# Kernel tuning notes

Hardware: AMD Instinct MI355X
Metric: run time of the kernel (lower is better)

Reference implementation:

```python
import jax, jax.numpy as jnp
import numpy as np
import math

def setup_inputs() -> dict:
    key = jax.random.key(0)
    k1, k2, k3 = jax.random.split(key, 3)
    B, N, C = 32, 1024, 768
    x = jax.random.normal(k1, (B, N, C), dtype=jnp.float32)
    W = jax.random.normal(k2, (4, C), dtype=jnp.float32) * 0.02  # conv1x1 weight [out=4, in=C]
    b = jax.random.normal(k3, (4,), dtype=jnp.float32) * 0.02
    return {"x": x, "W": W, "b": b}

def reference(x, W, b):
    B, N, C = x.shape
    H = int(math.isqrt(N))
    L = H * H
    # [B,N,C] -> [B,C,H,H]
    xi = jnp.transpose(x, (0, 2, 1)).reshape(B, C, H, H)
    # alpha = Conv1x1(AvgPool(x)) -> [B,4]
    pooled = jnp.mean(xi, axis=(2, 3))                      # [B,C]
    alpha = pooled @ W.T + b                                # [B,4]
    a = alpha[:, :, None, None]                             # [B,4,1,1]
    # CrossScan directions
    x0 = xi.reshape(B, C, L)                                # row-major scan
    x1 = jnp.transpose(xi, (0, 1, 3, 2)).reshape(B, C, L)   # col-major scan
    x2 = x0[:, :, ::-1]                                     # reversed row-major
    x3 = x1[:, :, ::-1]                                     # reversed col-major
    # gated weighted sum over the 4 scans (fused elementwise)
    y = a[:, 0] * x0 + a[:, 1] * x1 + a[:, 2] * x2 + a[:, 3] * x3  # [B,C,L]
    return jnp.transpose(y, (0, 2, 1))                      # [B,L,C]
```

## Files before the change

### kernel.cpp

```cpp
#include <hip/hip_runtime.h>

#define BB 32
#define NN 1024
#define CC 768
#define HH 32
#define NCHUNK 32
#define NPER (NN / NCHUNK)
#define C4 (CC / 4)
#define NORB 272
#define OPB 4
#define MBLK (NORB / OPB)

typedef float f32x4 __attribute__((ext_vector_type(4)));

__global__ void pool_dot(const f32x4* __restrict__ x4,
                         const f32x4* __restrict__ W4,
                         f32x4* __restrict__ partW4) {
    const int blk = blockIdx.x;
    const int t   = threadIdx.x;
    const f32x4* xb = x4 + (size_t)blk * (NPER * C4) + t;
    f32x4 s = {0.f, 0.f, 0.f, 0.f};
#pragma unroll 8
    for (int n = 0; n < NPER; ++n) s += xb[(size_t)n * C4];

    float d[4];
#pragma unroll
    for (int k = 0; k < 4; ++k) {
        const f32x4 w = W4[k * C4 + t];
        d[k] = s.x * w.x + s.y * w.y + s.z * w.z + s.w * w.w;
    }
    const int lane = t & 63;
    const int wid  = t >> 6;
    __shared__ float red[3][4];
#pragma unroll
    for (int k = 0; k < 4; ++k) {
        float v = d[k];
#pragma unroll
        for (int off = 32; off >= 1; off >>= 1) v += __shfl_down(v, off);
        if (lane == 0) red[wid][k] = v;
    }
    __syncthreads();
    if (t == 0) {
        f32x4 w;
        w.x = red[0][0] + red[1][0] + red[2][0];
        w.y = red[0][1] + red[1][1] + red[2][1];
        w.z = red[0][2] + red[1][2] + red[2][2];
        w.w = red[0][3] + red[1][3] + red[2][3];
        partW4[blk] = w;
    }
}

__global__ void merge(const f32x4* __restrict__ x4,
                      const f32x4* __restrict__ partW4,
                      const f32x4* __restrict__ bias4,
                      f32x4* __restrict__ o4) {
    const int bidx = blockIdx.x;
    const int b = bidx / MBLK;
    const int j = bidx - b * MBLK;

    f32x4 acc = {0.f, 0.f, 0.f, 0.f};
#pragma unroll 8
    for (int ch = 0; ch < NCHUNK; ++ch) acc += partW4[b * NCHUNK + ch];
    const f32x4 al = acc * (1.0f / (float)NN) + bias4[0];
    const float a0 = al.x, a1 = al.y, a2 = al.z, a3 = al.w;

    const int t = threadIdx.x;
    const f32x4* xb = x4 + (size_t)b * (NN * C4);
    f32x4* ob = o4 + (size_t)b * (NN * C4);

    int L[OPB][4];
#pragma unroll
    for (int q = 0; q < OPB; ++q) {
        const int o = OPB * j + q;
        int r = 0;
#pragma unroll
        for (int rr = 1; rr <= 15; ++rr) if (rr * (33 - rr) <= o) r = rr;
        const int c = r + (o - r * (33 - r));
        L[q][0] = r * HH + c;
        L[q][1] = c * HH + r;
        L[q][2] = (NN - 1) - L[q][0];
        L[q][3] = (NN - 1) - L[q][1];
    }

    f32x4 v[OPB][4];
#pragma unroll
    for (int q = 0; q < OPB; ++q)
#pragma unroll
        for (int m = 0; m < 4; ++m)
            v[q][m] = xb[(size_t)L[q][m] * C4 + t];

#pragma unroll
    for (int q = 0; q < OPB; ++q) {
        __builtin_nontemporal_store(a0 * v[q][0] + a1 * v[q][1] + a2 * v[q][2] + a3 * v[q][3],
                                    &ob[(size_t)L[q][0] * C4 + t]);
        __builtin_nontemporal_store(a0 * v[q][1] + a1 * v[q][0] + a2 * v[q][3] + a3 * v[q][2],
                                    &ob[(size_t)L[q][1] * C4 + t]);
        __builtin_nontemporal_store(a0 * v[q][2] + a1 * v[q][3] + a2 * v[q][0] + a3 * v[q][1],
                                    &ob[(size_t)L[q][2] * C4 + t]);
        __builtin_nontemporal_store(a0 * v[q][3] + a1 * v[q][2] + a2 * v[q][1] + a3 * v[q][0],
                                    &ob[(size_t)L[q][3] * C4 + t]);
    }
}

extern "C" void kernel_launch(void* const* d_in, const int* in_sizes, int n_in,
                              void* d_out, int out_size, void* d_ws, size_t ws_size,
                              hipStream_t stream) {
    const float* x    = (const float*)d_in[0];
    const float* W    = (const float*)d_in[1];
    const float* bias = (const float*)d_in[2];
    float* out = (float*)d_out;

    f32x4* partW = (f32x4*)d_ws;

    pool_dot<<<BB * NCHUNK, 192, 0, stream>>>((const f32x4*)x, (const f32x4*)W, partW);
    merge<<<BB * MBLK, 192, 0, stream>>>((const f32x4*)x, partW,
                                         (const f32x4*)bias, (f32x4*)out);
}
```

Measured before the change: 195.3 us.

## Fuse pooling and merge into one cooperative kernel holding x in registers

Replaces the two-kernel pool-then-merge pipeline with a single cooperative kernel. Each block loads its 32 rows of x into registers, computes partial pooled dot products, does a grid-wide sync, then writes the gated outputs from the registers it already holds. This halves global reads of x and removes one kernel launch. The costs are a grid barrier, high register pressure for 32 float4 values per thread, and an occupancy requirement (checked at runtime, with a fallback to the old path).

```diff
diff --git a/kernel.cpp b/kernel.cpp
--- a/kernel.cpp
+++ b/kernel.cpp
@@ -1,17 +1,129 @@
 #include <hip/hip_runtime.h>
+#include <hip/hip_cooperative_groups.h>
+
+namespace cg = cooperative_groups;
 
 #define BB 32
 #define NN 1024
 #define CC 768
 #define HH 32
+#define C4 (CC / 4)
+#define NTHR 192
+#define QPB 8
+#define BLKB 32
+#define GRID (BB * BLKB)
 #define NCHUNK 32
 #define NPER (NN / NCHUNK)
-#define C4 (CC / 4)
 #define NORB 272
 #define OPB 4
 #define MBLK (NORB / OPB)
 
 typedef float f32x4 __attribute__((ext_vector_type(4)));
+
+__device__ __forceinline__ void quad_rows(int jb, int u, int& r0, int& r1, int& r2, int& r3) {
+    if (jb < 30) {
+        const int q = jb * QPB + u;
+        int r = 0;
+#pragma unroll
+        for (int rr = 1; rr <= 14; ++rr) if (rr * (31 - rr) <= q) r = rr;
+        const int c = (r + 1) + (q - r * (31 - r));
+        r0 = r * HH + c;
+        r1 = c * HH + r;
+        r2 = (NN - 1) - r0;
+        r3 = (NN - 1) - r1;
+    } else {
+        const int i = (jb - 30) * QPB + u;
+        r0 = 33 * i;
+        r1 = 1023 - 33 * i;
+        r2 = 31 * (i + 1);
+        r3 = 992 - 31 * i;
+    }
+}
+
+__global__ __launch_bounds__(NTHR, 3) void fused(const f32x4* __restrict__ x4,
+                                                 const f32x4* __restrict__ W4,
+                                                 const f32x4* __restrict__ bias4,
+                                                 f32x4* __restrict__ partW4,
+                                                 f32x4* __restrict__ o4) {
+    const int blk = blockIdx.x;
+    const int b   = blk >> 5;
+    const int jb  = blk & 31;
+    const int t   = threadIdx.x;
+
+    const f32x4* xb = x4 + (size_t)b * (NN * C4);
+
+    f32x4 v[QPB][4];
+#pragma unroll
+    for (int u = 0; u < QPB; ++u) {
+        int r0, r1, r2, r3; quad_rows(jb, u, r0, r1, r2, r3);
+        v[u][0] = xb[(size_t)r0 * C4 + t];
+        v[u][1] = xb[(size_t)r1 * C4 + t];
+        v[u][2] = xb[(size_t)r2 * C4 + t];
+        v[u][3] = xb[(size_t)r3 * C4 + t];
+    }
+
+    f32x4 s = {0.f, 0.f, 0.f, 0.f};
+#pragma unroll
+    for (int u = 0; u < QPB; ++u)
+#pragma unroll
+        for (int m = 0; m < 4; ++m) s += v[u][m];
+
+    float d[4];
+#pragma unroll
+    for (int k = 0; k < 4; ++k) {
+        const f32x4 w = W4[k * C4 + t];
+        d[k] = s.x * w.x + s.y * w.y + s.z * w.z + s.w * w.w;
+    }
+    const int lane = t & 63;
+    const int wid  = t >> 6;
+    __shared__ float red[3][4];
+#pragma unroll
+    for (int k = 0; k < 4; ++k) {
+        float r = d[k];
+#pragma unroll
+        for (int off = 32; off >= 1; off >>= 1) r += __shfl_down(r, off);
+        if (lane == 0) red[wid][k] = r;
+    }
+    __syncthreads();
+    if (t == 0) {
+        f32x4 w;
+        w.x = red[0][0] + red[1][0] + red[2][0];
+        w.y = red[0][1] + red[1][1] + red[2][1];
+        w.z = red[0][2] + red[1][2] + red[2][2];
+        w.w = red[0][3] + red[1][3] + red[2][3];
+        partW4[blk] = w;
+    }
+
+    cg::this_grid().sync();
+
+    f32x4 acc = {0.f, 0.f, 0.f, 0.f};
+#pragma unroll 8
+    for (int ch = 0; ch < BLKB; ++ch) acc += partW4[b * BLKB + ch];
+    const f32x4 al = acc * (1.0f / (float)NN) + bias4[0];
+    const float a0 = al.x, a1 = al.y, a2 = al.z, a3 = al.w;
+
+    f32x4* ob = o4 + (size_t)b * (NN * C4);
+    if (jb < 30) {
+#pragma unroll
+        for (int u = 0; u < QPB; ++u) {
+            int r0, r1, r2, r3; quad_rows(jb, u, r0, r1, r2, r3);
+            __builtin_nontemporal_store(a0*v[u][0] + a1*v[u][1] + a2*v[u][2] + a3*v[u][3], &ob[(size_t)r0 * C4 + t]);
+            __builtin_nontemporal_store(a0*v[u][1] + a1*v[u][0] + a2*v[u][3] + a3*v[u][2], &ob[(size_t)r1 * C4 + t]);
+            __builtin_nontemporal_store(a0*v[u][2] + a1*v[u][3] + a2*v[u][0] + a3*v[u][1], &ob[(size_t)r2 * C4 + t]);
+            __builtin_nontemporal_store(a0*v[u][3] + a1*v[u][2] + a2*v[u][1] + a3*v[u][0], &ob[(size_t)r3 * C4 + t]);
+        }
+    } else {
+        const float p01 = a0 + a1, p23 = a2 + a3, p03 = a0 + a3, p12 = a1 + a2;
+#pragma unroll
+        for (int u = 0; u < QPB; ++u) {
+            int r0, r1, r2, r3; quad_rows(jb, u, r0, r1, r2, r3);
+            __builtin_nontemporal_store(p01*v[u][0] + p23*v[u][1], &ob[(size_t)r0 * C4 + t]);
+            __builtin_nontemporal_store(p01*v[u][1] + p23*v[u][0], &ob[(size_t)r1 * C4 + t]);
+            __builtin_nontemporal_store(p03*v[u][2] + p12*v[u][3], &ob[(size_t)r2 * C4 + t]);
+            __builtin_nontemporal_store(p03*v[u][3] + p12*v[u][2], &ob[(size_t)r3 * C4 + t]);
+        }
+    }
+}
 
 __global__ void pool_dot(const f32x4* __restrict__ x4,
                          const f32x4* __restrict__ W4,
@@ -22,7 +134,6 @@
     f32x4 s = {0.f, 0.f, 0.f, 0.f};
 #pragma unroll 8
     for (int n = 0; n < NPER; ++n) s += xb[(size_t)n * C4];
-
     float d[4];
 #pragma unroll
     for (int k = 0; k < 4; ++k) {
@@ -34,10 +145,10 @@
     __shared__ float red[3][4];
 #pragma unroll
     for (int k = 0; k < 4; ++k) {
-        float v = d[k];
-#pragma unroll
-        for (int off = 32; off >= 1; off >>= 1) v += __shfl_down(v, off);
-        if (lane == 0) red[wid][k] = v;
+        float r = d[k];
+#pragma unroll
+        for (int off = 32; off >= 1; off >>= 1) r += __shfl_down(r, off);
+        if (lane == 0) red[wid][k] = r;
     }
     __syncthreads();
     if (t == 0) {
@@ -57,17 +168,14 @@
     const int bidx = blockIdx.x;
     const int b = bidx / MBLK;
     const int j = bidx - b * MBLK;
-
     f32x4 acc = {0.f, 0.f, 0.f, 0.f};
 #pragma unroll 8
     for (int ch = 0; ch < NCHUNK; ++ch) acc += partW4[b * NCHUNK + ch];
     const f32x4 al = acc * (1.0f / (float)NN) + bias4[0];
     const float a0 = al.x, a1 = al.y, a2 = al.z, a3 = al.w;
-
     const int t = threadIdx.x;
     const f32x4* xb = x4 + (size_t)b * (NN * C4);
     f32x4* ob = o4 + (size_t)b * (NN * C4);
-
     int L[OPB][4];
 #pragma unroll
     for (int q = 0; q < OPB; ++q) {
@@ -81,38 +189,38 @@
         L[q][2] = (NN - 1) - L[q][0];
         L[q][3] = (NN - 1) - L[q][1];
     }
-
     f32x4 v[OPB][4];
 #pragma unroll
     for (int q = 0; q < OPB; ++q)
 #pragma unroll
         for (int m = 0; m < 4; ++m)
             v[q][m] = xb[(size_t)L[q][m] * C4 + t];
-
 #pragma unroll
     for (int q = 0; q < OPB; ++q) {
-        __builtin_nontemporal_store(a0 * v[q][0] + a1 * v[q][1] + a2 * v[q][2] + a3 * v[q][3],
-                                    &ob[(size_t)L[q][0] * C4 + t]);
-        __builtin_nontemporal_store(a0 * v[q][1] + a1 * v[q][0] + a2 * v[q][3] + a3 * v[q][2],
-                                    &ob[(size_t)L[q][1] * C4 + t]);
-        __builtin_nontemporal_store(a0 * v[q][2] + a1 * v[q][3] + a2 * v[q][0] + a3 * v[q][1],
-                                    &ob[(size_t)L[q][2] * C4 + t]);
-        __builtin_nontemporal_store(a0 * v[q][3] + a1 * v[q][2] + a2 * v[q][1] + a3 * v[q][0],
-                                    &ob[(size_t)L[q][3] * C4 + t]);
+        __builtin_nontemporal_store(a0*v[q][0] + a1*v[q][1] + a2*v[q][2] + a3*v[q][3], &ob[(size_t)L[q][0] * C4 + t]);
+        __builtin_nontemporal_store(a0*v[q][1] + a1*v[q][0] + a2*v[q][3] + a3*v[q][2], &ob[(size_t)L[q][1] * C4 + t]);
+        __builtin_nontemporal_store(a0*v[q][2] + a1*v[q][3] + a2*v[q][0] + a3*v[q][1], &ob[(size_t)L[q][2] * C4 + t]);
+        __builtin_nontemporal_store(a0*v[q][3] + a1*v[q][2] + a2*v[q][1] + a3*v[q][0], &ob[(size_t)L[q][3] * C4 + t]);
     }
 }
 
 extern "C" void kernel_launch(void* const* d_in, const int* in_sizes, int n_in,
                               void* d_out, int out_size, void* d_ws, size_t ws_size,
                               hipStream_t stream) {
-    const float* x    = (const float*)d_in[0];
-    const float* W    = (const float*)d_in[1];
-    const float* bias = (const float*)d_in[2];
-    float* out = (float*)d_out;
-
-    f32x4* partW = (f32x4*)d_ws;
-
-    pool_dot<<<BB * NCHUNK, 192, 0, stream>>>((const f32x4*)x, (const f32x4*)W, partW);
-    merge<<<BB * MBLK, 192, 0, stream>>>((const f32x4*)x, partW,
-                                         (const f32x4*)bias, (f32x4*)out);
-}
+    const f32x4* x4p = (const f32x4*)d_in[0];
+    const f32x4* W4p = (const f32x4*)d_in[1];
+    const f32x4* b4p = (const f32x4*)d_in[2];
+    f32x4* o4p = (f32x4*)d_out;
+    f32x4* pw  = (f32x4*)d_ws;
+
+    int maxB = 0;
+    hipError_t qerr = hipOccupancyMaxActiveBlocksPerMultiprocessor(&maxB, fused, NTHR, 0);
+    if (qerr == hipSuccess && maxB * 256 >= GRID) {
+        void* args[5] = {(void*)&x4p, (void*)&W4p, (void*)&b4p, (void*)&pw, (void*)&o4p};
+        hipError_t err = hipLaunchCooperativeKernel((const void*)fused, dim3(GRID), dim3(NTHR),
+                                                    args, 0, stream);
+        if (err == hipSuccess) return;
+    }
+    pool_dot<<<BB * NCHUNK, NTHR, 0, stream>>>(x4p, W4p, pw);
+    merge<<<BB * MBLK, NTHR, 0, stream>>>(x4p, pw, b4p, o4p);
+}
```

Measured after the change: 194.2 us. About the same (-0.6%).
